# Performance work log

Hardware: AMD Instinct MI355X
Metric: run time of the kernel (lower is better)

## Reference

```python
import jax, jax.numpy as jnp
import numpy as np

B, L, D_MODEL, D_STATE, D_CONV, EXPAND = 2, 1024, 1024, 16, 4, 2
D_INNER = D_MODEL * EXPAND


def setup_inputs() -> dict:
    key = jax.random.key(0)
    ks = jax.random.split(key, 8)
    s = lambda fan: 1.0 / np.sqrt(fan)
    x = jax.random.normal(ks[0], (B, L, D_MODEL), jnp.float32)
    in_proj_w = jax.random.normal(ks[1], (D_MODEL, 2 * D_INNER), jnp.float32) * s(D_MODEL)
    conv_w = jax.random.normal(ks[2], (D_INNER, 1, D_CONV), jnp.float32) * s(D_CONV)
    conv_b = jax.random.normal(ks[3], (D_INNER,), jnp.float32) * 0.01
    x_proj_w = jax.random.normal(ks[4], (D_INNER, 2 * D_STATE + D_INNER), jnp.float32) * s(D_INNER)
    dt_proj_w = jax.random.normal(ks[5], (D_INNER, D_INNER), jnp.float32) * s(D_INNER)
    dt_proj_b = jax.random.normal(ks[6], (D_INNER,), jnp.float32) * 0.01
    A_log = jnp.log(jnp.tile(jnp.arange(1, D_STATE + 1, dtype=jnp.float32)[None, :], (D_INNER, 1)))
    D = jnp.ones((D_INNER,), jnp.float32)
    out_proj_w = jax.random.normal(ks[7], (D_INNER, D_MODEL), jnp.float32) * s(D_INNER)
    return {"x": x, "in_proj_w": in_proj_w, "conv_w": conv_w, "conv_b": conv_b,
            "x_proj_w": x_proj_w, "dt_proj_w": dt_proj_w, "dt_proj_b": dt_proj_b,
            "A_log": A_log, "D": D, "out_proj_w": out_proj_w}


def _mamba_forward(x, in_proj_w, conv_w, conv_b, x_proj_w, dt_proj_w, dt_proj_b, A_log, D, out_proj_w):
    Bb, Ll, _ = x.shape
    d_inner, _, d_conv = conv_w.shape
    d_state = A_log.shape[1]
    # input projection and gate split
    xz = x @ in_proj_w                       # [B, L, 2*Di]
    x_inner, z = jnp.split(xz, 2, axis=-1)   # each [B, L, Di]
    # causal depthwise conv (left pad k-1, truncate to L == torch pad+slice)
    xc = jnp.transpose(x_inner, (0, 2, 1))   # [B, Di, L]
    xc = jax.lax.conv_general_dilated(
        xc, conv_w, window_strides=(1,), padding=[(d_conv - 1, 0)],
        dimension_numbers=("NCH", "OIH", "NCH"), feature_group_count=d_inner)
    xc = xc + conv_b[None, :, None]
    u = jax.nn.silu(jnp.transpose(xc, (0, 2, 1)))  # [B, L, Di]
    # SSM parameter projections
    ssm = u @ x_proj_w                        # [B, L, 2N+Di]
    B_ssm = ssm[..., :d_state]                # [B, L, N]
    C_ssm = ssm[..., d_state:2 * d_state]     # [B, L, N]
    dt = jax.nn.softplus(ssm[..., 2 * d_state:] @ dt_proj_w + dt_proj_b)  # [B, L, Di]
    A_real = -jnp.exp(A_log)                  # [Di, N]
    # selective scan over sequence (recurrence via lax.scan)
    def step(h, inp):
        dt_t, B_t, u_t = inp                  # [B,Di], [B,N], [B,Di]
        dA = jnp.exp(dt_t[..., None] * A_real)            # [B, Di, N]
        dBu = dt_t[..., None] * B_t[:, None, :] * u_t[..., None]
        h = dA * h + dBu
        return h, h
    h0 = jnp.zeros((Bb, d_inner, d_state), x.dtype)
    xs = (jnp.swapaxes(dt, 0, 1), jnp.swapaxes(B_ssm, 0, 1), jnp.swapaxes(u, 0, 1))
    _, states = jax.lax.scan(step, h0, xs)    # [L, B, Di, N]
    y = jnp.einsum("lbdn,lbn->lbd", states, jnp.swapaxes(C_ssm, 0, 1))
    y = jnp.swapaxes(y, 0, 1) + D * u         # skip connection
    y = y * jax.nn.silu(z)                    # gating
    return y @ out_proj_w                     # [B, L, d_model]


def reference(x, in_proj_w, conv_w, conv_b, x_proj_w, dt_proj_w, dt_proj_b, A_log, D, out_proj_w):
    return _mamba_forward(x, in_proj_w, conv_w, conv_b, x_proj_w, dt_proj_w, dt_proj_b, A_log, D, out_proj_w)
```

## Files before the change

kernel.cpp:

```cpp
#include <hip/hip_runtime.h>
#include <hip/hip_bf16.h>

#define BB 2
#define LL 1024
#define DMODEL 1024
#define DINNER 2048
#define DSTATE 16
#define DCONV 4
#define MM (BB * LL)
#define N_XZ 4096
#define N_SSM 2080
#define N_SSM_PAD 2176
#define CCH 32
#define LCH 32

typedef __hip_bfloat16 bf16;
typedef short bf16x8 __attribute__((ext_vector_type(8)));
typedef float f32x4 __attribute__((ext_vector_type(4)));

__device__ __forceinline__ void load16_lds(const bf16* g, bf16* l) {
    __builtin_amdgcn_global_load_lds(
        (const __attribute__((address_space(1))) void*)g,
        (__attribute__((address_space(3))) void*)l,
        16, 0, 0);
}

__global__ __launch_bounds__(256) void prep_kernel(
    const float* __restrict__ x, bf16* __restrict__ xbf,
    const float* __restrict__ w1, bf16* __restrict__ o1,
    const float* __restrict__ w3, bf16* __restrict__ o3,
    const float* __restrict__ w4, bf16* __restrict__ o4,
    const float* __restrict__ w2, bf16* __restrict__ w2bf,
    bf16* __restrict__ w2bc)
{
    int bid = blockIdx.x;
    if (bid >= 14464) {
        bid -= 14464;
        int i = (bid * 256 + threadIdx.x) * 4;
        float4 v = *(const float4*)(x + i);
        xbf[i + 0] = __float2bfloat16(v.x);
        xbf[i + 1] = __float2bfloat16(v.y);
        xbf[i + 2] = __float2bfloat16(v.z);
        xbf[i + 3] = __float2bfloat16(v.w);
        return;
    }
    if (bid >= 10240 && bid < 14400) {
        bid -= 10240;
        int i = (bid * 256 + threadIdx.x) * 4;
        float4 v = *(const float4*)(w2 + i);
        w2bf[i + 0] = __float2bfloat16(v.x);
        w2bf[i + 1] = __float2bfloat16(v.y);
        w2bf[i + 2] = __float2bfloat16(v.z);
        w2bf[i + 3] = __float2bfloat16(v.w);
        return;
    }
    const float* src; bf16* dst; int K, N, tn, tk, srcld;
    if (bid < 4096)        { src = w1; dst = o1; K = 1024; N = 4096; tn = bid & 127; tk = bid >> 7; srcld = N; }
    else if (bid < 8192)   { bid -= 4096; src = w3; dst = o3; K = 2048; N = 2048; tn = bid & 63; tk = bid >> 6; srcld = N; }
    else if (bid < 10240)  { bid -= 8192; src = w4; dst = o4; K = 2048; N = 1024; tn = bid & 31; tk = bid >> 5; srcld = N; }
    else                   { bid -= 14400; src = w2; dst = w2bc; K = 2048; N = 32; tn = 0; tk = bid; srcld = N_SSM; }
    __shared__ float tile[32][33];
    const int nb = tn * 32, kb = tk * 32;
    const int tx = threadIdx.x & 31, ty = threadIdx.x >> 5;
    #pragma unroll
    for (int i = 0; i < 32; i += 8) {
        int k = kb + ty + i, n = nb + tx;
        tile[ty + i][tx] = (k < K && n < N) ? src[(size_t)k * srcld + n] : 0.f;
    }
    __syncthreads();
    #pragma unroll
    for (int i = 0; i < 32; i += 8) {
        int n = nb + ty + i, k = kb + tx;
        if (n < N && k < K) dst[(size_t)n * K + k] = __float2bfloat16(tile[tx][ty + i]);
    }
}

#define TM 128
#define TN 64
#define TK 64

template<int SWZ>
__device__ __forceinline__ void remap(int id, int NX, int& bx, int& by) {
    if (SWZ >= 0) {
        int xcd = id & 7, slot = id >> 3;
        bx = (xcd << SWZ) + (slot & ((1 << SWZ) - 1));
        by = slot >> SWZ;
    } else { bx = id % NX; by = id / NX; }
}

template<int EPI>
__device__ __forceinline__ void gemm_body(
    bf16* AsB, bf16* BsB, int bx, int by,
    const bf16* __restrict__ A, int lda,
    const bf16* __restrict__ Wt, int ldw,
    float* __restrict__ Cf, bf16* __restrict__ Cb, int ldc,
    const float* __restrict__ bias,
    int N, int K, int kbeg, int Kc, bool at)
{
    const int tid = threadIdx.x;
    const int wave = tid >> 6, lane = tid & 63;
    const int wm = (wave >> 1) * 64, wn = (wave & 1) * 32;
    const int m0 = by * TM, n0 = bx * TN;
    const int lm = lane & 15, kq = lane >> 4;

    const int srow = lane >> 3;
    const int schunk = (lane & 7) ^ srow;
    const bf16* gA = A + (size_t)(m0 + wave * 32 + srow) * lda + schunk * 8;
    const bf16* gB = Wt + (size_t)(n0 + wave * 16 + srow) * ldw + schunk * 8;

    const int NK = Kc / TK;
    f32x4 acc[4][2] = {};
    const int fsw = (lm & 7);

    auto stage = [&](int buf, int it) {
        const int k0 = kbeg + it * TK;
        bf16* lA = AsB + buf * (TM * TK) + (wave * 32) * TK;
        bf16* lB = BsB + buf * (TN * TK) + (wave * 16) * TK;
        #pragma unroll
        for (int g = 0; g < 4; ++g)
            load16_lds(gA + (size_t)(8 * g) * lda + k0, lA + (8 * g) * TK);
        #pragma unroll
        for (int g = 0; g < 2; ++g)
            load16_lds(gB + (size_t)(8 * g) * ldw + k0, lB + (8 * g) * TK);
    };
    auto compute = [&](int buf) {
        const bf16* Asb = AsB + buf * (TM * TK);
        const bf16* Bsb = BsB + buf * (TN * TK);
        bf16x8 af[4][2], bfr[2][2];
        #pragma unroll
        for (int i = 0; i < 4; ++i)
            #pragma unroll
            for (int t = 0; t < 2; ++t)
                af[i][t] = *(const bf16x8*)(&Asb[(wm + i * 16 + lm) * TK + ((t * 4 + kq) ^ fsw) * 8]);
        #pragma unroll
        for (int j = 0; j < 2; ++j)
            #pragma unroll
            for (int t = 0; t < 2; ++t)
                bfr[j][t] = *(const bf16x8*)(&Bsb[(wn + j * 16 + lm) * TK + ((t * 4 + kq) ^ fsw) * 8]);
        #pragma unroll
        for (int t = 0; t < 2; ++t)
            #pragma unroll
            for (int i = 0; i < 4; ++i)
                #pragma unroll
                for (int j = 0; j < 2; ++j)
                    acc[i][j] = __builtin_amdgcn_mfma_f32_16x16x32_bf16(af[i][t], bfr[j][t], acc[i][j], 0, 0, 0);
    };

    stage(0, 0);
    for (int it = 0; it < NK; it += 2) {
        stage(1, it + 1);
        __builtin_amdgcn_s_waitcnt(0x0F76);
        __builtin_amdgcn_s_barrier();
        compute(0);
        __builtin_amdgcn_s_barrier();
        if (it + 2 < NK) {
            stage(0, it + 2);
            __builtin_amdgcn_s_waitcnt(0x0F76);
        } else {
            __builtin_amdgcn_s_waitcnt(0x0F70);
        }
        __builtin_amdgcn_s_barrier();
        compute(1);
        __builtin_amdgcn_s_barrier();
    }

    #pragma unroll
    for (int i = 0; i < 4; ++i) {
        #pragma unroll
        for (int j = 0; j < 2; ++j) {
            int gcol = n0 + wn + j * 16 + lm;
            if ((EPI == 0 || EPI == 3) && gcol >= N) continue;
            #pragma unroll
            for (int r = 0; r < 4; ++r) {
                int grow = m0 + wm + i * 16 + kq * 4 + r;
                float v = acc[i][j][r];
                if (EPI == 1) {
                    v += bias[gcol];
                    v = (v > 20.f) ? v : log1pf(__expf(v));
                    Cf[(size_t)grow * ldc + gcol] = v;
                } else if (EPI == 2) {
                    if (at) atomicAdd(&Cf[(size_t)grow * ldc + gcol], v);
                    else    Cf[(size_t)grow * ldc + gcol] = v;
                } else if (EPI == 3) {
                    if (gcol < 32) Cf[(size_t)grow * 32 + gcol] = v;
                    else           Cb[(size_t)grow * ldc + gcol] = __float2bfloat16(v);
                } else {
                    Cb[(size_t)grow * ldc + gcol] = __float2bfloat16(v);
                }
            }
        }
    }
}

template<int EPI, int KSPLIT = 1, int SWZ = -1>
__global__ __launch_bounds__(256) void mfma_gemm(
    const bf16* __restrict__ A, int lda,
    const bf16* __restrict__ Wt, int ldw,
    float* __restrict__ Cf, bf16* __restrict__ Cb, int ldc,
    const float* __restrict__ bias,
    int N, int K)
{
    __shared__ __align__(16) bf16 As[2][TM * TK];
    __shared__ __align__(16) bf16 Bs[2][TN * TK];
    int bx, by;
    if (SWZ >= 0) {
        int id = blockIdx.x + (int)(gridDim.x * blockIdx.y);
        remap<SWZ>(id, gridDim.x, bx, by);
    } else { bx = blockIdx.x; by = blockIdx.y; }
    const int Kc = K / KSPLIT;
    const int kbeg = (KSPLIT > 1) ? blockIdx.z * Kc : 0;
    gemm_body<EPI>(&As[0][0], &Bs[0][0], bx, by, A, lda, Wt, ldw, Cf, Cb, ldc,
                   bias, N, K, kbeg, Kc, KSPLIT > 1);
}

template<int EPI0, int SWZ0, int EPI1, int SWZ1>
__global__ __launch_bounds__(256) void mfma_gemm_dual(
    int nblk0, int NX0,
    const bf16* __restrict__ A0, int lda0, const bf16* __restrict__ Wt0, int ldw0,
    float* __restrict__ Cf0, bf16* __restrict__ Cb0, int ldc0,
    const float* __restrict__ bias0, int N0, int K0,
    int NX1,
    const bf16* __restrict__ A1, int lda1, const bf16* __restrict__ Wt1, int ldw1,
    float* __restrict__ Cf1, bf16* __restrict__ Cb1, int ldc1,
    const float* __restrict__ bias1, int N1, int K1)
{
    __shared__ __align__(16) bf16 As[2][TM * TK];
    __shared__ __align__(16) bf16 Bs[2][TN * TK];
    int id = blockIdx.x;
    if (id < nblk0) {
        int bx, by; remap<SWZ0>(id, NX0, bx, by);
        gemm_body<EPI0>(&As[0][0], &Bs[0][0], bx, by, A0, lda0, Wt0, ldw0,
                        Cf0, Cb0, ldc0, bias0, N0, K0, 0, K0, false);
    } else {
        id -= nblk0;
        int bx, by; remap<SWZ1>(id, NX1, bx, by);
        gemm_body<EPI1>(&As[0][0], &Bs[0][0], bx, by, A1, lda1, Wt1, ldw1,
                        Cf1, Cb1, ldc1, bias1, N1, K1, 0, K1, false);
    }
}

__global__ void conv_silu_kernel(const bf16* __restrict__ xz,
                                 const float* __restrict__ conv_w,
                                 const float* __restrict__ conv_b,
                                 bf16* __restrict__ u)
{
    int idx = blockIdx.x * blockDim.x + threadIdx.x;
    int d8 = idx & (DINNER / 8 - 1);
    int l  = (idx >> 8) & (LL - 1);
    int b  = idx >> 18;
    int d0 = d8 * 8;

    float acc[8];
    {
        float4 b0 = *(const float4*)(conv_b + d0);
        float4 b1 = *(const float4*)(conv_b + d0 + 4);
        acc[0] = b0.x; acc[1] = b0.y; acc[2] = b0.z; acc[3] = b0.w;
        acc[4] = b1.x; acc[5] = b1.y; acc[6] = b1.z; acc[7] = b1.w;
    }
    #pragma unroll
    for (int j = 0; j < DCONV; ++j) {
        int ll = l - (DCONV - 1) + j;
        if (ll >= 0) {
            bf16x8 v = *(const bf16x8*)(xz + ((size_t)(b * LL + ll)) * N_XZ + d0);
            #pragma unroll
            for (int r = 0; r < 8; ++r) {
                float xv = __uint_as_float(((unsigned)(unsigned short)v[r]) << 16);
                acc[r] = fmaf(conv_w[(d0 + r) * DCONV + j], xv, acc[r]);
            }
        }
    }
    bf16x8 out;
    #pragma unroll
    for (int r = 0; r < 8; ++r) {
        float y = acc[r] / (1.f + __expf(-acc[r]));
        bf16 h = __float2bfloat16(y);
        out[r] = *reinterpret_cast<short*>(&h);
    }
    *(bf16x8*)(u + ((size_t)(b * LL + l)) * DINNER + d0) = out;
}

__global__ __launch_bounds__(256) void scan_phase_a(
    const float* __restrict__ dt, const bf16* __restrict__ u,
    const float* __restrict__ BC,
    const float* __restrict__ A_log,
    float* __restrict__ chunkP, float* __restrict__ chunkH)
{
    const int d = blockIdx.x * 256 + threadIdx.x;
    const int c = blockIdx.y, b = blockIdx.z;
    const int l0 = c * LCH;

    float A[DSTATE];
    {
        const f32x4* ap = (const f32x4*)(A_log + d * DSTATE);
        #pragma unroll
        for (int q = 0; q < 4; ++q) {
            f32x4 v = ap[q];
            #pragma unroll
            for (int r = 0; r < 4; ++r) A[q * 4 + r] = -__expf(v[r]);
        }
    }
    float h[DSTATE];
    #pragma unroll
    for (int n = 0; n < DSTATE; ++n) h[n] = 0.f;
    float sdt = 0.f;

    const float* dtp = dt + ((size_t)b * LL + l0) * DINNER + d;
    const bf16* up = u + ((size_t)b * LL + l0) * DINNER + d;
    const float* bcp = BC + ((size_t)b * LL + l0) * 32;

    #pragma unroll 2
    for (int i = 0; i < LCH; ++i) {
        float dtv = *dtp;
        float uv  = (float)*up;
        float du  = dtv * uv;
        f32x4 Bv[4];
        #pragma unroll
        for (int q = 0; q < 4; ++q) Bv[q] = *(const f32x4*)(bcp + q * 4);
        #pragma unroll
        for (int n = 0; n < DSTATE; ++n) {
            float a = __expf(dtv * A[n]);
            h[n] = fmaf(a, h[n], du * Bv[n >> 2][n & 3]);
        }
        sdt += dtv;
        dtp += DINNER; up += DINNER; bcp += 32;
    }

    size_t idx = (((size_t)b * CCH + c) * DINNER + d) * DSTATE;
    #pragma unroll
    for (int q = 0; q < 4; ++q) {
        f32x4 pv, hv;
        #pragma unroll
        for (int r = 0; r < 4; ++r) { pv[r] = __expf(A[q * 4 + r] * sdt); hv[r] = h[q * 4 + r]; }
        *(f32x4*)(chunkP + idx + q * 4) = pv;
        *(f32x4*)(chunkH + idx + q * 4) = hv;
    }
}

__global__ __launch_bounds__(256) void scan_phase_p(
    const float* __restrict__ chunkP, float* __restrict__ chunkH)
{
    int gid = blockIdx.x * 256 + threadIdx.x;
    int n = gid & 15;
    int d = (gid >> 4) & (DINNER - 1);
    int b = gid >> 15;
    const size_t stride = (size_t)DINNER * DSTATE;
    size_t idx = ((size_t)b * CCH * DINNER + d) * DSTATE + n;
    float H = 0.f;
    for (int c = 0; c < CCH; ++c) {
        float P  = chunkP[idx];
        float hl = chunkH[idx];
        chunkH[idx] = H;
        H = fmaf(P, H, hl);
        idx += stride;
    }
}

__global__ __launch_bounds__(256) void scan_phase_b(
    const float* __restrict__ dt, bf16* __restrict__ u,
    const float* __restrict__ BC, const bf16* __restrict__ xz,
    const float* __restrict__ A_log, const float* __restrict__ Dp,
    const float* __restrict__ chunkH)
{
    const int d = blockIdx.x * 256 + threadIdx.x;
    const int c = blockIdx.y, b = blockIdx.z;
    const int l0 = c * LCH;

    float A[DSTATE];
    {
        const f32x4* ap = (const f32x4*)(A_log + d * DSTATE);
        #pragma unroll
        for (int q = 0; q < 4; ++q) {
            f32x4 v = ap[q];
            #pragma unroll
            for (int r = 0; r < 4; ++r) A[q * 4 + r] = -__expf(v[r]);
        }
    }
    const float Dd = Dp[d];
    float h[DSTATE];
    {
        size_t idx = (((size_t)b * CCH + c) * DINNER + d) * DSTATE;
        #pragma unroll
        for (int q = 0; q < 4; ++q) {
            f32x4 v = *(const f32x4*)(chunkH + idx + q * 4);
            #pragma unroll
            for (int r = 0; r < 4; ++r) h[q * 4 + r] = v[r];
        }
    }

    const float* dtp = dt + ((size_t)b * LL + l0) * DINNER + d;
    bf16* up = u + ((size_t)b * LL + l0) * DINNER + d;
    const float* bcp = BC + ((size_t)b * LL + l0) * 32;
    const bf16* zp = xz + ((size_t)b * LL + l0) * N_XZ + DINNER + d;

    #pragma unroll 2
    for (int i = 0; i < LCH; ++i) {
        float dtv = *dtp;
        float uv  = (float)*up;
        float du  = dtv * uv;
        f32x4 Bv[4], Cv[4];
        #pragma unroll
        for (int q = 0; q < 4; ++q) {
            Bv[q] = *(const f32x4*)(bcp + q * 4);
            Cv[q] = *(const f32x4*)(bcp + 16 + q * 4);
        }
        float acc = 0.f;
        #pragma unroll
        for (int n = 0; n < DSTATE; ++n) {
            float a = __expf(dtv * A[n]);
            h[n] = fmaf(a, h[n], du * Bv[n >> 2][n & 3]);
            acc = fmaf(h[n], Cv[n >> 2][n & 3], acc);
        }
        float zv = (float)*zp;
        acc = fmaf(Dd, uv, acc);
        acc *= zv / (1.f + __expf(-zv));
        *up = __float2bfloat16(acc);
        dtp += DINNER; up += DINNER; bcp += 32; zp += N_XZ;
    }
}

extern "C" void kernel_launch(void* const* d_in, const int* in_sizes, int n_in,
                              void* d_out, int out_size, void* d_ws, size_t ws_size,
                              hipStream_t stream) {
    const float* x         = (const float*)d_in[0];
    const float* in_proj_w = (const float*)d_in[1];
    const float* conv_w    = (const float*)d_in[2];
    const float* conv_b    = (const float*)d_in[3];
    const float* x_proj_w  = (const float*)d_in[4];
    const float* dt_proj_w = (const float*)d_in[5];
    const float* dt_proj_b = (const float*)d_in[6];
    const float* A_log     = (const float*)d_in[7];
    const float* Dp        = (const float*)d_in[8];
    const float* out_proj_w= (const float*)d_in[9];
    float* out = (float*)d_out;

    char* p = (char*)d_ws;
    float* dt   = (float*)p;                          p += (size_t)MM * DINNER * 4;
    bf16*  xbf  = (bf16*)dt;
    bf16*  xz   = (bf16*)p;                           p += (size_t)MM * N_XZ * 2;
    bf16*  u    = (bf16*)p;                           p += (size_t)MM * DINNER * 2;
    bf16*  wft  = (bf16*)p;                           p += (size_t)MM * N_SSM * 2;
    bf16*  Wt1  = (bf16*)p;                           p += (size_t)N_XZ * DMODEL * 2;
    bf16*  w2slot = (bf16*)p;                         p += (size_t)N_SSM_PAD * DINNER * 2;
    bf16*  W2bf = w2slot;
    bf16*  w2bc = w2slot + (size_t)DINNER * N_SSM;
    bf16*  Wt3  = (bf16*)p;                           p += (size_t)DINNER * DINNER * 2;
    bf16*  Wt4  = (bf16*)p;                           p += (size_t)DMODEL * DINNER * 2;
    float* BC   = (float*)p;                          p += (size_t)MM * 32 * 4;
    float* chunkP = (float*)Wt1;
    float* chunkH = (float*)w2slot;

    prep_kernel<<<16512, 256, 0, stream>>>(x, xbf, in_proj_w, Wt1, dt_proj_w, Wt3,
                                           out_proj_w, Wt4, x_proj_w, W2bf, w2bc);
    mfma_gemm_dual<0, 3, 0, 2><<<1536, 256, 0, stream>>>(
        1024, 64, xbf, DMODEL, Wt1, DMODEL, nullptr, xz, N_XZ, nullptr, N_XZ, DMODEL,
        32, Wt3, DINNER, W2bf + 32, N_SSM, nullptr, wft, DINNER, nullptr, DINNER, DINNER);
    {
        int n = BB * LL * DINNER / 8;
        conv_silu_kernel<<<(n + 255) / 256, 256, 0, stream>>>(xz, conv_w, conv_b, u);
    }
    mfma_gemm_dual<1, 2, 3, -1><<<528, 256, 0, stream>>>(
        512, 32, u, DINNER, wft, DINNER, dt, nullptr, DINNER, dt_proj_b, DINNER, DINNER,
        1, u, DINNER, w2bc, DINNER, BC, nullptr, 32, nullptr, 32, DINNER);
    scan_phase_a<<<dim3(DINNER / 256, CCH, BB), 256, 0, stream>>>(dt, u, BC, A_log, chunkP, chunkH);
    scan_phase_p<<<dim3(BB * DINNER * DSTATE / 256), 256, 0, stream>>>(chunkP, chunkH);
    scan_phase_b<<<dim3(DINNER / 256, CCH, BB), 256, 0, stream>>>(dt, u, BC, xz, A_log, Dp, chunkH);
    hipMemsetAsync(out, 0, (size_t)out_size * sizeof(float), stream);
    mfma_gemm<2, 4, 1><<<dim3(DMODEL / TN, MM / TM, 4), 256, 0, stream>>>(
        u, DINNER, Wt4, DINNER, out, nullptr, DMODEL, nullptr, DMODEL, DINNER);
}
```

Before: 334.2 us.

## Widen GEMM tiles to 128x128, split-K the dt GEMM, move softplus into scan

Enlarges the GEMM block tile from 128x64 to 128x128 so each wave computes a 64x64 sub-tile, raising MFMA work per LDS load and halving block counts. The dt-projection GEMM becomes split-K with atomic accumulation into a zeroed buffer, so the bias+softplus epilogue moves into both scan phases where dt is read. Dual-GEMM launches are reordered and regrouped, adding split-K support and a separate dt memset. The cost is more registers and LDS per block, fewer blocks for occupancy, extra atomics and a memset, and softplus computed twice per element across the two scan phases.

```diff
diff --git a/kernel.cpp b/kernel.cpp
--- a/kernel.cpp
+++ b/kernel.cpp
@@ -25,6 +25,15 @@
         16, 0, 0);
 }
 
+template<int SWZ>
+__device__ __forceinline__ void remap(int id, int NX, int& bx, int& by) {
+    if (SWZ >= 0) {
+        int xcd = id & 7, slot = id >> 3;
+        bx = (xcd << SWZ) + (slot & ((1 << SWZ) - 1));
+        by = slot >> SWZ;
+    } else { bx = id % NX; by = id / NX; }
+}
+
 __global__ __launch_bounds__(256) void prep_kernel(
     const float* __restrict__ x, bf16* __restrict__ xbf,
     const float* __restrict__ w1, bf16* __restrict__ o1,
@@ -76,17 +85,8 @@
 }
 
 #define TM 128
-#define TN 64
+#define TN 128
 #define TK 64
-
-template<int SWZ>
-__device__ __forceinline__ void remap(int id, int NX, int& bx, int& by) {
-    if (SWZ >= 0) {
-        int xcd = id & 7, slot = id >> 3;
-        bx = (xcd << SWZ) + (slot & ((1 << SWZ) - 1));
-        by = slot >> SWZ;
-    } else { bx = id % NX; by = id / NX; }
-}
 
 template<int EPI>
 __device__ __forceinline__ void gemm_body(
@@ -99,41 +99,40 @@
 {
     const int tid = threadIdx.x;
     const int wave = tid >> 6, lane = tid & 63;
-    const int wm = (wave >> 1) * 64, wn = (wave & 1) * 32;
+    const int wm = (wave >> 1) * 64, wn = (wave & 1) * 64;
     const int m0 = by * TM, n0 = bx * TN;
     const int lm = lane & 15, kq = lane >> 4;
 
     const int srow = lane >> 3;
     const int schunk = (lane & 7) ^ srow;
-    const bf16* gA = A + (size_t)(m0 + wave * 32 + srow) * lda + schunk * 8;
-    const bf16* gB = Wt + (size_t)(n0 + wave * 16 + srow) * ldw + schunk * 8;
+    const bf16* gA = A  + (size_t)(m0 + wave * 32 + srow) * lda + schunk * 8;
+    const bf16* gB = Wt + (size_t)(n0 + wave * 32 + srow) * ldw + schunk * 8;
 
     const int NK = Kc / TK;
-    f32x4 acc[4][2] = {};
-    const int fsw = (lm & 7);
+    f32x4 acc[4][4] = {};
+    const int fsw = lm & 7;
 
     auto stage = [&](int buf, int it) {
         const int k0 = kbeg + it * TK;
         bf16* lA = AsB + buf * (TM * TK) + (wave * 32) * TK;
-        bf16* lB = BsB + buf * (TN * TK) + (wave * 16) * TK;
-        #pragma unroll
-        for (int g = 0; g < 4; ++g)
+        bf16* lB = BsB + buf * (TN * TK) + (wave * 32) * TK;
+        #pragma unroll
+        for (int g = 0; g < 4; ++g) {
             load16_lds(gA + (size_t)(8 * g) * lda + k0, lA + (8 * g) * TK);
-        #pragma unroll
-        for (int g = 0; g < 2; ++g)
             load16_lds(gB + (size_t)(8 * g) * ldw + k0, lB + (8 * g) * TK);
+        }
     };
     auto compute = [&](int buf) {
         const bf16* Asb = AsB + buf * (TM * TK);
         const bf16* Bsb = BsB + buf * (TN * TK);
-        bf16x8 af[4][2], bfr[2][2];
+        bf16x8 af[4][2], bfr[4][2];
         #pragma unroll
         for (int i = 0; i < 4; ++i)
             #pragma unroll
             for (int t = 0; t < 2; ++t)
                 af[i][t] = *(const bf16x8*)(&Asb[(wm + i * 16 + lm) * TK + ((t * 4 + kq) ^ fsw) * 8]);
         #pragma unroll
-        for (int j = 0; j < 2; ++j)
+        for (int j = 0; j < 4; ++j)
             #pragma unroll
             for (int t = 0; t < 2; ++t)
                 bfr[j][t] = *(const bf16x8*)(&Bsb[(wn + j * 16 + lm) * TK + ((t * 4 + kq) ^ fsw) * 8]);
@@ -142,20 +141,20 @@
             #pragma unroll
             for (int i = 0; i < 4; ++i)
                 #pragma unroll
-                for (int j = 0; j < 2; ++j)
+                for (int j = 0; j < 4; ++j)
                     acc[i][j] = __builtin_amdgcn_mfma_f32_16x16x32_bf16(af[i][t], bfr[j][t], acc[i][j], 0, 0, 0);
     };
 
     stage(0, 0);
     for (int it = 0; it < NK; it += 2) {
         stage(1, it + 1);
-        __builtin_amdgcn_s_waitcnt(0x0F76);
+        __builtin_amdgcn_s_waitcnt(0x0F78);
         __builtin_amdgcn_s_barrier();
         compute(0);
         __builtin_amdgcn_s_barrier();
         if (it + 2 < NK) {
             stage(0, it + 2);
-            __builtin_amdgcn_s_waitcnt(0x0F76);
+            __builtin_amdgcn_s_waitcnt(0x0F78);
         } else {
             __builtin_amdgcn_s_waitcnt(0x0F70);
         }
@@ -167,7 +166,7 @@
     #pragma unroll
     for (int i = 0; i < 4; ++i) {
         #pragma unroll
-        for (int j = 0; j < 2; ++j) {
+        for (int j = 0; j < 4; ++j) {
             int gcol = n0 + wn + j * 16 + lm;
             if ((EPI == 0 || EPI == 3) && gcol >= N) continue;
             #pragma unroll
@@ -182,8 +181,7 @@
                     if (at) atomicAdd(&Cf[(size_t)grow * ldc + gcol], v);
                     else    Cf[(size_t)grow * ldc + gcol] = v;
                 } else if (EPI == 3) {
-                    if (gcol < 32) Cf[(size_t)grow * 32 + gcol] = v;
-                    else           Cb[(size_t)grow * ldc + gcol] = __float2bfloat16(v);
+                    Cf[(size_t)grow * 32 + gcol] = v;
                 } else {
                     Cb[(size_t)grow * ldc + gcol] = __float2bfloat16(v);
                 }
@@ -193,15 +191,15 @@
 }
 
 template<int EPI, int KSPLIT = 1, int SWZ = -1>
-__global__ __launch_bounds__(256) void mfma_gemm(
+__global__ __launch_bounds__(256, 2) void mfma_gemm(
     const bf16* __restrict__ A, int lda,
     const bf16* __restrict__ Wt, int ldw,
     float* __restrict__ Cf, bf16* __restrict__ Cb, int ldc,
     const float* __restrict__ bias,
     int N, int K)
 {
-    __shared__ __align__(16) bf16 As[2][TM * TK];
-    __shared__ __align__(16) bf16 Bs[2][TN * TK];
+    __shared__ __align__(16) bf16 As[2 * TM * TK];
+    __shared__ __align__(16) bf16 Bs[2 * TN * TK];
     int bx, by;
     if (SWZ >= 0) {
         int id = blockIdx.x + (int)(gridDim.x * blockIdx.y);
@@ -209,12 +207,12 @@
     } else { bx = blockIdx.x; by = blockIdx.y; }
     const int Kc = K / KSPLIT;
     const int kbeg = (KSPLIT > 1) ? blockIdx.z * Kc : 0;
-    gemm_body<EPI>(&As[0][0], &Bs[0][0], bx, by, A, lda, Wt, ldw, Cf, Cb, ldc,
+    gemm_body<EPI>(As, Bs, bx, by, A, lda, Wt, ldw, Cf, Cb, ldc,
                    bias, N, K, kbeg, Kc, KSPLIT > 1);
 }
 
-template<int EPI0, int SWZ0, int EPI1, int SWZ1>
-__global__ __launch_bounds__(256) void mfma_gemm_dual(
+template<int EPI0, int KS0, int SWZ0, int EPI1, int KS1, int SWZ1>
+__global__ __launch_bounds__(256, 2) void mfma_gemm_dual(
     int nblk0, int NX0,
     const bf16* __restrict__ A0, int lda0, const bf16* __restrict__ Wt0, int ldw0,
     float* __restrict__ Cf0, bf16* __restrict__ Cb0, int ldc0,
@@ -224,18 +222,24 @@
     float* __restrict__ Cf1, bf16* __restrict__ Cb1, int ldc1,
     const float* __restrict__ bias1, int N1, int K1)
 {
-    __shared__ __align__(16) bf16 As[2][TM * TK];
-    __shared__ __align__(16) bf16 Bs[2][TN * TK];
+    __shared__ __align__(16) bf16 As[2 * TM * TK];
+    __shared__ __align__(16) bf16 Bs[2 * TN * TK];
     int id = blockIdx.x;
     if (id < nblk0) {
-        int bx, by; remap<SWZ0>(id, NX0, bx, by);
-        gemm_body<EPI0>(&As[0][0], &Bs[0][0], bx, by, A0, lda0, Wt0, ldw0,
-                        Cf0, Cb0, ldc0, bias0, N0, K0, 0, K0, false);
+        int kz = (KS0 > 1) ? id % KS0 : 0;
+        int tl = (KS0 > 1) ? id / KS0 : id;
+        int bx, by; remap<SWZ0>(tl, NX0, bx, by);
+        const int Kc = K0 / KS0;
+        gemm_body<EPI0>(As, Bs, bx, by, A0, lda0, Wt0, ldw0,
+                        Cf0, Cb0, ldc0, bias0, N0, K0, kz * Kc, Kc, KS0 > 1);
     } else {
         id -= nblk0;
-        int bx, by; remap<SWZ1>(id, NX1, bx, by);
-        gemm_body<EPI1>(&As[0][0], &Bs[0][0], bx, by, A1, lda1, Wt1, ldw1,
-                        Cf1, Cb1, ldc1, bias1, N1, K1, 0, K1, false);
+        int kz = (KS1 > 1) ? id % KS1 : 0;
+        int tl = (KS1 > 1) ? id / KS1 : id;
+        int bx, by; remap<SWZ1>(tl, NX1, bx, by);
+        const int Kc = K1 / KS1;
+        gemm_body<EPI1>(As, Bs, bx, by, A1, lda1, Wt1, ldw1,
+                        Cf1, Cb1, ldc1, bias1, N1, K1, kz * Kc, Kc, KS1 > 1);
     }
 }
 
@@ -281,8 +285,8 @@
 
 __global__ __launch_bounds__(256) void scan_phase_a(
     const float* __restrict__ dt, const bf16* __restrict__ u,
-    const float* __restrict__ BC,
-    const float* __restrict__ A_log,
+    const float* __restrict__ BC, const float* __restrict__ A_log,
+    const float* __restrict__ dtb,
     float* __restrict__ chunkP, float* __restrict__ chunkH)
 {
     const int d = blockIdx.x * 256 + threadIdx.x;
@@ -299,6 +303,7 @@
             for (int r = 0; r < 4; ++r) A[q * 4 + r] = -__expf(v[r]);
         }
     }
+    const float bd = dtb[d];
     float h[DSTATE];
     #pragma unroll
     for (int n = 0; n < DSTATE; ++n) h[n] = 0.f;
@@ -310,7 +315,8 @@
 
     #pragma unroll 2
     for (int i = 0; i < LCH; ++i) {
-        float dtv = *dtp;
+        float dtv = *dtp + bd;
+        dtv = (dtv > 20.f) ? dtv : log1pf(__expf(dtv));
         float uv  = (float)*up;
         float du  = dtv * uv;
         f32x4 Bv[4];
@@ -359,6 +365,7 @@
     const float* __restrict__ dt, bf16* __restrict__ u,
     const float* __restrict__ BC, const bf16* __restrict__ xz,
     const float* __restrict__ A_log, const float* __restrict__ Dp,
+    const float* __restrict__ dtb,
     const float* __restrict__ chunkH)
 {
     const int d = blockIdx.x * 256 + threadIdx.x;
@@ -376,6 +383,7 @@
         }
     }
     const float Dd = Dp[d];
+    const float bd = dtb[d];
     float h[DSTATE];
     {
         size_t idx = (((size_t)b * CCH + c) * DINNER + d) * DSTATE;
@@ -394,7 +402,8 @@
 
     #pragma unroll 2
     for (int i = 0; i < LCH; ++i) {
-        float dtv = *dtp;
+        float dtv = *dtp + bd;
+        dtv = (dtv > 20.f) ? dtv : log1pf(__expf(dtv));
         float uv  = (float)*up;
         float du  = dtv * uv;
         f32x4 Bv[4], Cv[4];
@@ -451,20 +460,21 @@
 
     prep_kernel<<<16512, 256, 0, stream>>>(x, xbf, in_proj_w, Wt1, dt_proj_w, Wt3,
                                            out_proj_w, Wt4, x_proj_w, W2bf, w2bc);
-    mfma_gemm_dual<0, 3, 0, 2><<<1536, 256, 0, stream>>>(
-        1024, 64, xbf, DMODEL, Wt1, DMODEL, nullptr, xz, N_XZ, nullptr, N_XZ, DMODEL,
-        32, Wt3, DINNER, W2bf + 32, N_SSM, nullptr, wft, DINNER, nullptr, DINNER, DINNER);
+    mfma_gemm_dual<0, 1, 1, 0, 1, 2><<<768, 256, 0, stream>>>(
+        256, 16, Wt3, DINNER, W2bf + 32, N_SSM, nullptr, wft, DINNER, nullptr, DINNER, DINNER,
+        32, xbf, DMODEL, Wt1, DMODEL, nullptr, xz, N_XZ, nullptr, N_XZ, DMODEL);
+    hipMemsetAsync(dt, 0, (size_t)MM * DINNER * 4, stream);
+    hipMemsetAsync(out, 0, (size_t)out_size * sizeof(float), stream);
     {
         int n = BB * LL * DINNER / 8;
         conv_silu_kernel<<<(n + 255) / 256, 256, 0, stream>>>(xz, conv_w, conv_b, u);
     }
-    mfma_gemm_dual<1, 2, 3, -1><<<528, 256, 0, stream>>>(
-        512, 32, u, DINNER, wft, DINNER, dt, nullptr, DINNER, dt_proj_b, DINNER, DINNER,
-        1, u, DINNER, w2bc, DINNER, BC, nullptr, 32, nullptr, 32, DINNER);
-    scan_phase_a<<<dim3(DINNER / 256, CCH, BB), 256, 0, stream>>>(dt, u, BC, A_log, chunkP, chunkH);
+    mfma_gemm_dual<3, 1, -1, 2, 2, 1><<<528, 256, 0, stream>>>(
+        16, 1, u, DINNER, w2bc, DINNER, BC, nullptr, 32, nullptr, 32, DINNER,
+        16, u, DINNER, wft, DINNER, dt, nullptr, DINNER, nullptr, DINNER, DINNER);
+    scan_phase_a<<<dim3(DINNER / 256, CCH, BB), 256, 0, stream>>>(dt, u, BC, A_log, dt_proj_b, chunkP, chunkH);
     scan_phase_p<<<dim3(BB * DINNER * DSTATE / 256), 256, 0, stream>>>(chunkP, chunkH);
-    scan_phase_b<<<dim3(DINNER / 256, CCH, BB), 256, 0, stream>>>(dt, u, BC, xz, A_log, Dp, chunkH);
-    hipMemsetAsync(out, 0, (size_t)out_size * sizeof(float), stream);
-    mfma_gemm<2, 4, 1><<<dim3(DMODEL / TN, MM / TM, 4), 256, 0, stream>>>(
+    scan_phase_b<<<dim3(DINNER / 256, CCH, BB), 256, 0, stream>>>(dt, u, BC, xz, A_log, Dp, dt_proj_b, chunkH);
+    mfma_gemm<2, 4, 0><<<dim3(8, 16, 4), 256, 0, stream>>>(
         u, DINNER, Wt4, DINNER, out, nullptr, DMODEL, nullptr, DMODEL, DINNER);
 }
```

Result: slower. 383.0 us (+14.6%).
